# Kernel tuning notes

Hardware: AMD Instinct MI355X
Metric: run time of the kernel (lower is better)

Reference implementation:

```python
import jax, jax.numpy as jnp
import numpy as np

N_NODES = 100000
F_STATE = 64
HIDDEN = 256
N_EDGES = 1600000


def setup_inputs() -> dict:
    key = jax.random.key(0)
    ks = jax.random.split(key, 8)
    x = jax.random.normal(ks[0], (N_NODES, F_STATE), dtype=jnp.float32)
    edge_index = jax.random.randint(ks[1], (2, N_EDGES), 0, N_NODES, dtype=jnp.int32)
    # Pre-process MLP (1 layer): Dense(F_STATE -> HIDDEN), relu
    W_pre = jax.random.normal(ks[2], (F_STATE, HIDDEN), dtype=jnp.float32) / np.sqrt(F_STATE)
    b_pre = jnp.zeros((HIDDEN,), dtype=jnp.float32)
    # GeneralConv: Dense(HIDDEN -> HIDDEN), relu, then sum-aggregate message passing
    W_conv = jax.random.normal(ks[3], (HIDDEN, HIDDEN), dtype=jnp.float32) / np.sqrt(HIDDEN)
    b_conv = jnp.zeros((HIDDEN,), dtype=jnp.float32)
    # Post-process MLP (1 layer): Dense(2*HIDDEN -> F_STATE), activation=None
    W_post = jax.random.normal(ks[4], (2 * HIDDEN, F_STATE), dtype=jnp.float32) / np.sqrt(2 * HIDDEN)
    b_post = jnp.zeros((F_STATE,), dtype=jnp.float32)
    return {
        "x": x,
        "edge_index": edge_index,
        "W_pre": W_pre,
        "b_pre": b_pre,
        "W_conv": W_conv,
        "b_conv": b_conv,
        "W_post": W_post,
        "b_post": b_post,
        "steps": 4,
    }


def reference(x, edge_index, W_pre, b_pre, W_conv, b_conv, W_post, b_post, steps):
    n = x.shape[0]
    dst = edge_index[0]  # a.indices[:, 0] -> aggregation targets
    src = edge_index[1]  # a.indices[:, 1] -> message sources

    def step(h, _):
        p = jax.nn.relu(h @ W_pre + b_pre)                 # pre MLP     [N, H]
        m = jax.nn.relu(p @ W_conv + b_conv)               # conv dense  [N, H]
        z = jax.ops.segment_sum(m[src], dst, num_segments=n)  # sum agg  [N, H]
        out = jnp.concatenate([z, p], axis=-1) @ W_post + b_post  # cat-skip + post MLP (linear)
        return out, None

    out, _ = jax.lax.scan(step, x, None, length=steps)
    return out
```

## Files before the change

### kernel.cpp

```cpp
#include <hip/hip_runtime.h>


#define NN 100000
#define NPAD 100064
#define FS 64
#define HH 256
#define NE 1600000
#define NSTEPS 4
#define GA 128
#define EPB (NE / GA)
#define BK2SH 9
#define BS2 (1 << BK2SH)
#define NBK2 ((NN + BS2 - 1) / BS2)

typedef unsigned short u16;
typedef unsigned int u32;
typedef __attribute__((ext_vector_type(8))) short bfrag;
typedef __attribute__((ext_vector_type(4))) float ffrag;

static __device__ __forceinline__ u16 f2bf(float f) {
    union { float f; u32 u; } v; v.f = f;
    return (u16)((v.u + 0x7fffu + ((v.u >> 16) & 1u)) >> 16);
}
static __device__ __forceinline__ float bf2f(u16 h) {
    union { u32 u; float f; } v; v.u = (u32)h << 16; return v.f;
}
static __device__ __forceinline__ u32 pack2bf(float a, float b) {
    return (u32)f2bf(a) | ((u32)f2bf(b) << 16);
}

__global__ void cvt_x_k(const float4* __restrict__ x, uint2* __restrict__ hbf, int n4) {
    int i = blockIdx.x * 256 + threadIdx.x;
    if (i < n4) {
        float4 v = x[i];
        hbf[i] = make_uint2(pack2bf(v.x, v.y), pack2bf(v.z, v.w));
    }
}

__global__ void prep_w_k(const float* __restrict__ W_pre, const float* __restrict__ W_conv,
                         const float* __restrict__ W_post,
                         u16* __restrict__ Wpt, u16* __restrict__ Wct,
                         u16* __restrict__ Wzt, u16* __restrict__ Wp2t) {
    int i = blockIdx.x * 256 + threadIdx.x;
    if (i < 65536) {
        int c = i >> 8, k = i & 255;
        Wct[i] = f2bf(W_conv[k * HH + c]);
    } else if (i < 81920) {
        int j = i - 65536;
        int c = j >> 6, k = j & 63;
        Wpt[j] = f2bf(W_pre[k * HH + c]);
    } else if (i < 98304) {
        int j = i - 81920;
        int c = j >> 8, k = j & 255;
        Wzt[j] = f2bf(W_post[k * FS + c]);
    } else if (i < 114688) {
        int j = i - 98304;
        int c = j >> 8, k = j & 255;
        Wp2t[j] = f2bf(W_post[(HH + k) * FS + c]);
    }
}

__global__ __launch_bounds__(256) void fillA_k(const int* __restrict__ dst, const int* __restrict__ src,
                                               int* __restrict__ cntM, int* __restrict__ offM,
                                               u32* __restrict__ tmp) {
    __shared__ int cnt[256];
    __shared__ int sc[256];
    __shared__ int cur[256];
    const int t = threadIdx.x, b = blockIdx.x;
    const int e0 = b * EPB;
    cnt[t] = 0;
    __syncthreads();
    for (int i = t; i < EPB; i += 256) atomicAdd(&cnt[dst[e0 + i] >> BK2SH], 1);
    __syncthreads();
    int v = cnt[t];
    sc[t] = v;
    __syncthreads();
    for (int o = 1; o < 256; o <<= 1) {
        int y = (t >= o) ? sc[t - o] : 0;
        __syncthreads();
        sc[t] += y;
        __syncthreads();
    }
    int excl = sc[t] - v;
    cur[t] = excl;
    if (t < NBK2) {
        cntM[t * GA + b] = v;
        offM[t * GA + b] = excl;
    }
    __syncthreads();
    u32* seg = tmp + (size_t)b * EPB;
    for (int i = t; i < EPB; i += 256) {
        int d = dst[e0 + i], s = src[e0 + i];
        int pos = atomicAdd(&cur[d >> BK2SH], 1);
        seg[pos] = ((u32)(d & (BS2 - 1)) << 23) | (u32)s;
    }
}

__global__ void bscan_k(const int* __restrict__ cntM, int* __restrict__ bstart) {
    __shared__ int sh[256];
    const int t = threadIdx.x;
    int tot = 0;
    if (t < NBK2)
        for (int b = 0; b < GA; b++) tot += cntM[t * GA + b];
    sh[t] = tot;
    __syncthreads();
    for (int o = 1; o < 256; o <<= 1) {
        int y = (t >= o) ? sh[t - o] : 0;
        __syncthreads();
        sh[t] += y;
        __syncthreads();
    }
    if (t < NBK2) bstart[t] = sh[t] - tot;
    if (t == 255) bstart[NBK2] = sh[255];
}

__global__ __launch_bounds__(256) void fillB_k(const u32* __restrict__ tmp,
                                               const int* __restrict__ cntM, const int* __restrict__ offM,
                                               const int* __restrict__ bstart,
                                               int* __restrict__ offsets, int* __restrict__ srcs) {
    __shared__ int cnt[BS2];
    __shared__ int cur[BS2];
    __shared__ int runlen[GA];
    __shared__ int runoff[GA];
    const int t = threadIdx.x, k = blockIdx.x;
    const int nodeBase = k << BK2SH;
    cnt[t] = 0;
    cnt[t + 256] = 0;
    if (t < GA) {
        runlen[t] = cntM[k * GA + t];
        runoff[t] = offM[k * GA + t];
    }
    __syncthreads();
    const int rsub = t >> 6;
    const int elane = t & 63;
    for (int g = 0; g < GA / 4; g++) {
        int rb = g * 4 + rsub;
        int len = runlen[rb];
        const u32* run = tmp + (size_t)rb * EPB + runoff[rb];
        for (int e = elane; e < len; e += 64) atomicAdd(&cnt[run[e] >> 23], 1);
    }
    __syncthreads();
    int a = cnt[2 * t], b2 = cnt[2 * t + 1];
    int s = a + b2;
    cur[t] = s;
    __syncthreads();
    for (int o = 1; o < 256; o <<= 1) {
        int y = (t >= o) ? cur[t - o] : 0;
        __syncthreads();
        cur[t] += y;
        __syncthreads();
    }
    int exclPair = cur[t] - s;
    __syncthreads();
    const int base = bstart[k];
    int o0 = base + exclPair;
    int o1 = o0 + a;
    int n0 = nodeBase + 2 * t, n1 = n0 + 1;
    if (n0 < NN) offsets[n0] = o0;
    if (n1 < NN) offsets[n1] = o1;
    cur[2 * t] = o0;
    cur[2 * t + 1] = o1;
    __syncthreads();
    for (int g = 0; g < GA / 4; g++) {
        int rb = g * 4 + rsub;
        int len = runlen[rb];
        const u32* run = tmp + (size_t)rb * EPB + runoff[rb];
        for (int e = elane; e < len; e += 64) {
            u32 p = run[e];
            int pos = atomicAdd(&cur[p >> 23], 1);
            srcs[pos] = (int)(p & 0x7FFFFFu);
        }
    }
}

__global__ void final_off_k(int* __restrict__ offsets) {
    if (threadIdx.x == 0) offsets[NN] = NE;
}

__global__ __launch_bounds__(256, 3) void xform_k(const u16* __restrict__ hbf,
                                                  const u16* __restrict__ Wpt,
                                                  const float* __restrict__ b_pre,
                                                  const u16* __restrict__ Wct,
                                                  const float* __restrict__ b_conv,
                                                  const u16* __restrict__ Wzt,
                                                  const u16* __restrict__ Wp2t,
                                                  u16* __restrict__ qbf,
                                                  u16* __restrict__ pw2o) {
    __shared__ __align__(16) u16 ts[64 * 264];
    __shared__ __align__(16) u16 stA[64 * 72];
    __shared__ __align__(16) u16 stB[64 * 72];
    const int t = threadIdx.x;
    const int wave = t >> 6, lane = t & 63;
    const int quad = lane >> 4, l16 = lane & 15;
    const int nodeBase = blockIdx.x * 64;

    {
        ffrag acc[4][4];
#pragma unroll
        for (int mt = 0; mt < 4; mt++)
#pragma unroll
            for (int nt = 0; nt < 4; nt++) acc[mt][nt] = (ffrag)0.f;
#pragma unroll
        for (int ch = 0; ch < 2; ch++) {
            const int kb = ch * 32 + quad * 8;
            bfrag a[4], b[4];
#pragma unroll
            for (int mt = 0; mt < 4; mt++)
                a[mt] = *(const bfrag*)(hbf + (size_t)(nodeBase + mt * 16 + l16) * FS + kb);
#pragma unroll
            for (int nt = 0; nt < 4; nt++)
                b[nt] = *(const bfrag*)(Wpt + (size_t)(wave * 64 + nt * 16 + l16) * FS + kb);
#pragma unroll
            for (int mt = 0; mt < 4; mt++)
#pragma unroll
                for (int nt = 0; nt < 4; nt++)
                    acc[mt][nt] = __builtin_amdgcn_mfma_f32_16x16x32_bf16(a[mt], b[nt], acc[mt][nt], 0, 0, 0);
        }
#pragma unroll
        for (int nt = 0; nt < 4; nt++) {
            const int col = wave * 64 + nt * 16 + l16;
            const float bv = b_pre[col];
#pragma unroll
            for (int mt = 0; mt < 4; mt++)
#pragma unroll
                for (int r = 0; r < 4; r++)
                    ts[(mt * 16 + quad * 4 + r) * 264 + col] = f2bf(fmaxf(acc[mt][nt][r] + bv, 0.f));
        }
    }
    __syncthreads();

    ffrag accm[4][4];
    ffrag accw[4];
    {
#pragma unroll
        for (int mt = 0; mt < 4; mt++) {
            accw[mt] = (ffrag)0.f;
#pragma unroll
            for (int nt = 0; nt < 4; nt++) accm[mt][nt] = (ffrag)0.f;
        }
        bfrag b[2][4], bw[2];
        {
            const int kb0 = quad * 8;
#pragma unroll
            for (int nt = 0; nt < 4; nt++)
                b[0][nt] = *(const bfrag*)(Wct + (size_t)(wave * 64 + nt * 16 + l16) * HH + kb0);
            bw[0] = *(const bfrag*)(Wp2t + (size_t)(wave * 16 + l16) * HH + kb0);
        }
#pragma unroll
        for (int ch = 0; ch < 8; ch++) {
            const int cur = ch & 1, nxt = cur ^ 1;
            if (ch < 7) {
                const int kb2 = (ch + 1) * 32 + quad * 8;
#pragma unroll
                for (int nt = 0; nt < 4; nt++)
                    b[nxt][nt] = *(const bfrag*)(Wct + (size_t)(wave * 64 + nt * 16 + l16) * HH + kb2);
                bw[nxt] = *(const bfrag*)(Wp2t + (size_t)(wave * 16 + l16) * HH + kb2);
            }
            const int kb = ch * 32 + quad * 8;
            bfrag a[4];
#pragma unroll
            for (int mt = 0; mt < 4; mt++)
                a[mt] = *(const bfrag*)(ts + (mt * 16 + l16) * 264 + kb);
#pragma unroll
            for (int mt = 0; mt < 4; mt++) {
#pragma unroll
                for (int nt = 0; nt < 4; nt++)
                    accm[mt][nt] = __builtin_amdgcn_mfma_f32_16x16x32_bf16(a[mt], b[cur][nt], accm[mt][nt], 0, 0, 0);
                accw[mt] = __builtin_amdgcn_mfma_f32_16x16x32_bf16(a[mt], bw[cur], accw[mt], 0, 0, 0);
            }
        }
    }
    __syncthreads();

    {
#pragma unroll
        for (int nt = 0; nt < 4; nt++) {
            const int col = wave * 64 + nt * 16 + l16;
            const float bv = b_conv[col];
#pragma unroll
            for (int mt = 0; mt < 4; mt++)
#pragma unroll
                for (int r = 0; r < 4; r++)
                    ts[(mt * 16 + quad * 4 + r) * 264 + col] = f2bf(fmaxf(accm[mt][nt][r] + bv, 0.f));
        }
        const int colw = wave * 16 + l16;
#pragma unroll
        for (int mt = 0; mt < 4; mt++)
#pragma unroll
            for (int r = 0; r < 4; r++)
                stA[(mt * 16 + quad * 4 + r) * 72 + colw] = f2bf(accw[mt][r]);
    }
    __syncthreads();

#pragma unroll
    for (int s = 0; s < 2; s++) {
        const int j = t + s * 256;
        const int row = j >> 3, seg = j & 7;
        uint4 v = *(const uint4*)(stA + row * 72 + seg * 8);
        *(uint4*)(pw2o + (size_t)(nodeBase + row) * FS + seg * 8) = v;
    }

    {
        ffrag qa[4];
#pragma unroll
        for (int mt = 0; mt < 4; mt++) qa[mt] = (ffrag)0.f;
        bfrag bz[2];
        bz[0] = *(const bfrag*)(Wzt + (size_t)(wave * 16 + l16) * HH + quad * 8);
#pragma unroll
        for (int ch = 0; ch < 8; ch++) {
            const int cur = ch & 1;
            if (ch < 7)
                bz[cur ^ 1] = *(const bfrag*)(Wzt + (size_t)(wave * 16 + l16) * HH + (ch + 1) * 32 + quad * 8);
            const int kb = ch * 32 + quad * 8;
#pragma unroll
            for (int mt = 0; mt < 4; mt++) {
                bfrag am = *(const bfrag*)(ts + (mt * 16 + l16) * 264 + kb);
                qa[mt] = __builtin_amdgcn_mfma_f32_16x16x32_bf16(am, bz[cur], qa[mt], 0, 0, 0);
            }
        }
        const int col = wave * 16 + l16;
#pragma unroll
        for (int mt = 0; mt < 4; mt++)
#pragma unroll
            for (int r = 0; r < 4; r++)
                stB[(mt * 16 + quad * 4 + r) * 72 + col] = f2bf(qa[mt][r]);
    }
    __syncthreads();

#pragma unroll
    for (int s = 0; s < 2; s++) {
        const int j = t + s * 256;
        const int row = j >> 3, seg = j & 7;
        uint4 v = *(const uint4*)(stB + row * 72 + seg * 8);
        *(uint4*)(qbf + (size_t)(nodeBase + row) * FS + seg * 8) = v;
    }
}

__global__ __launch_bounds__(256) void agg_k(const u32* __restrict__ q2,
                                             const int* __restrict__ offsets,
                                             const int* __restrict__ srcs,
                                             const u32* __restrict__ pw2,
                                             const float* __restrict__ b_post,
                                             u32* __restrict__ hbf_out,
                                             float* __restrict__ outf) {
    const int wave = threadIdx.x >> 6;
    const int lane = threadIdx.x & 63;
    const int node = blockIdx.x * 4 + wave;
    const int half = lane >> 5, c = lane & 31;
    const int beg = offsets[node], end = offsets[node + 1];
    float ax = 0.f, ay = 0.f, bx = 0.f, by = 0.f;
    int e = beg + half;
    for (; e + 6 < end; e += 8) {
        int s0 = srcs[e], s1 = srcs[e + 2], s2 = srcs[e + 4], s3 = srcs[e + 6];
        u32 g0 = q2[(size_t)s0 * 32 + c];
        u32 g1 = q2[(size_t)s1 * 32 + c];
        u32 g2 = q2[(size_t)s2 * 32 + c];
        u32 g3 = q2[(size_t)s3 * 32 + c];
        ax += bf2f((u16)g0) + bf2f((u16)g1);
        ay += bf2f((u16)(g0 >> 16)) + bf2f((u16)(g1 >> 16));
        bx += bf2f((u16)g2) + bf2f((u16)g3);
        by += bf2f((u16)(g2 >> 16)) + bf2f((u16)(g3 >> 16));
    }
    for (; e < end; e += 2) {
        u32 g = q2[(size_t)srcs[e] * 32 + c];
        ax += bf2f((u16)g);
        ay += bf2f((u16)(g >> 16));
    }
    ax += bx; ay += by;
    ax += __shfl_xor(ax, 32);
    ay += __shfl_xor(ay, 32);
    if (half == 0) {
        u32 wp = pw2[(size_t)node * 32 + c];
        float2 b = *(const float2*)&b_post[2 * c];
        float hx = ax + bf2f((u16)wp) + b.x;
        float hy = ay + bf2f((u16)(wp >> 16)) + b.y;
        if (outf) {
            *(float2*)&outf[(size_t)node * FS + 2 * c] = make_float2(hx, hy);
        } else {
            hbf_out[(size_t)node * 32 + c] = pack2bf(hx, hy);
        }
    }
}

extern "C" void kernel_launch(void* const* d_in, const int* in_sizes, int n_in,
                              void* d_out, int out_size, void* d_ws, size_t ws_size,
                              hipStream_t stream) {
    const float* x      = (const float*)d_in[0];
    const int*   ei     = (const int*)d_in[1];
    const float* W_pre  = (const float*)d_in[2];
    const float* b_pre  = (const float*)d_in[3];
    const float* W_conv = (const float*)d_in[4];
    const float* b_conv = (const float*)d_in[5];
    const float* W_post = (const float*)d_in[6];
    const float* b_post = (const float*)d_in[7];
    float* out = (float*)d_out;

    char* ws = (char*)d_ws;
    size_t off = 0;
    auto alloc = [&](size_t bytes) -> char* {
        char* r = ws + off;
        off += (bytes + 255) & ~(size_t)255;
        return r;
    };
    u16* hbf     = (u16*)alloc((size_t)NPAD * FS * 2);
    u16* qbf     = (u16*)alloc((size_t)NPAD * FS * 2);
    u16* pw2     = (u16*)alloc((size_t)NPAD * FS * 2);
    u32* tmp     = (u32*)alloc((size_t)NE * 4);
    int* offsets = (int*)alloc((size_t)(NN + 1) * 4);
    int* srcs    = (int*)alloc((size_t)NE * 4);
    int* cntM    = (int*)alloc((size_t)NBK2 * GA * 4);
    int* offM    = (int*)alloc((size_t)NBK2 * GA * 4);
    int* bstart  = (int*)alloc((size_t)(NBK2 + 1) * 4);
    u16* Wpt     = (u16*)alloc((size_t)HH * FS * 2);
    u16* Wct     = (u16*)alloc((size_t)HH * HH * 2);
    u16* Wzt     = (u16*)alloc((size_t)FS * HH * 2);
    u16* Wp2t    = (u16*)alloc((size_t)FS * HH * 2);
    (void)ws_size; (void)in_sizes; (void)n_in; (void)out_size;

    const int* dst = ei;
    const int* src = ei + NE;

    cvt_x_k<<<(NN * FS / 4 + 255) / 256, 256, 0, stream>>>((const float4*)x, (uint2*)hbf, NN * FS / 4);
    prep_w_k<<<448, 256, 0, stream>>>(W_pre, W_conv, W_post, Wpt, Wct, Wzt, Wp2t);

    fillA_k<<<GA, 256, 0, stream>>>(dst, src, cntM, offM, tmp);
    bscan_k<<<1, 256, 0, stream>>>(cntM, bstart);
    fillB_k<<<NBK2, 256, 0, stream>>>(tmp, cntM, offM, bstart, offsets, srcs);
    final_off_k<<<1, 64, 0, stream>>>(offsets);

    const int GB = (NN + 63) / 64;
    for (int s = 0; s < NSTEPS; s++) {
        xform_k<<<GB, 256, 0, stream>>>(hbf, Wpt, b_pre, Wct, b_conv, Wzt, Wp2t, qbf, pw2);
        if (s < NSTEPS - 1)
            agg_k<<<NN / 4, 256, 0, stream>>>((const u32*)qbf, offsets, srcs, (const u32*)pw2, b_post,
                                              (u32*)hbf, nullptr);
        else
            agg_k<<<NN / 4, 256, 0, stream>>>((const u32*)qbf, offsets, srcs, (const u32*)pw2, b_post,
                                              nullptr, out);
    }
}
```

Baseline: 607.6 us.

## Split xform tile across eight waves and deepen gather unroll in aggregation

The node-transform kernel moves from 4 to 8 waves per 64-node block. Each wave now computes 32 output columns instead of 64, and the small 64-wide projections are split by row-tile and column-half. This lowers per-wave register pressure and raises occupancy, but it drops the explicit double-buffered weight prefetch and adds a barrier around the shared staging buffer, which is now reused. The aggregation kernel also gains a 16-edge unrolled loop so more independent gathers are in flight per half-wave.

```diff
diff --git a/kernel.cpp b/kernel.cpp
--- a/kernel.cpp
+++ b/kernel.cpp
@@ -177,7 +177,7 @@
     if (threadIdx.x == 0) offsets[NN] = NE;
 }
 
-__global__ __launch_bounds__(256, 3) void xform_k(const u16* __restrict__ hbf,
+__global__ __launch_bounds__(512, 4) void xform_k(const u16* __restrict__ hbf,
                                                   const u16* __restrict__ Wpt,
                                                   const float* __restrict__ b_pre,
                                                   const u16* __restrict__ Wct,
@@ -187,38 +187,39 @@
                                                   u16* __restrict__ qbf,
                                                   u16* __restrict__ pw2o) {
     __shared__ __align__(16) u16 ts[64 * 264];
-    __shared__ __align__(16) u16 stA[64 * 72];
-    __shared__ __align__(16) u16 stB[64 * 72];
+    __shared__ __align__(16) u16 st[64 * 72];
     const int t = threadIdx.x;
     const int wave = t >> 6, lane = t & 63;
     const int quad = lane >> 4, l16 = lane & 15;
+    const int w4 = wave & 3;
+    const int wh = wave >> 2;
     const int nodeBase = blockIdx.x * 64;
 
     {
-        ffrag acc[4][4];
-#pragma unroll
-        for (int mt = 0; mt < 4; mt++)
-#pragma unroll
-            for (int nt = 0; nt < 4; nt++) acc[mt][nt] = (ffrag)0.f;
+        ffrag acc[4][2];
+#pragma unroll
+        for (int mt = 0; mt < 4; mt++) {
+            acc[mt][0] = (ffrag)0.f;
+            acc[mt][1] = (ffrag)0.f;
+        }
 #pragma unroll
         for (int ch = 0; ch < 2; ch++) {
             const int kb = ch * 32 + quad * 8;
-            bfrag a[4], b[4];
+            bfrag a[4], b0, b1;
 #pragma unroll
             for (int mt = 0; mt < 4; mt++)
                 a[mt] = *(const bfrag*)(hbf + (size_t)(nodeBase + mt * 16 + l16) * FS + kb);
-#pragma unroll
-            for (int nt = 0; nt < 4; nt++)
-                b[nt] = *(const bfrag*)(Wpt + (size_t)(wave * 64 + nt * 16 + l16) * FS + kb);
-#pragma unroll
-            for (int mt = 0; mt < 4; mt++)
-#pragma unroll
-                for (int nt = 0; nt < 4; nt++)
-                    acc[mt][nt] = __builtin_amdgcn_mfma_f32_16x16x32_bf16(a[mt], b[nt], acc[mt][nt], 0, 0, 0);
-        }
-#pragma unroll
-        for (int nt = 0; nt < 4; nt++) {
-            const int col = wave * 64 + nt * 16 + l16;
+            b0 = *(const bfrag*)(Wpt + (size_t)(wave * 32 + l16) * FS + kb);
+            b1 = *(const bfrag*)(Wpt + (size_t)(wave * 32 + 16 + l16) * FS + kb);
+#pragma unroll
+            for (int mt = 0; mt < 4; mt++) {
+                acc[mt][0] = __builtin_amdgcn_mfma_f32_16x16x32_bf16(a[mt], b0, acc[mt][0], 0, 0, 0);
+                acc[mt][1] = __builtin_amdgcn_mfma_f32_16x16x32_bf16(a[mt], b1, acc[mt][1], 0, 0, 0);
+            }
+        }
+#pragma unroll
+        for (int nt = 0; nt < 2; nt++) {
+            const int col = wave * 32 + nt * 16 + l16;
             const float bv = b_pre[col];
 #pragma unroll
             for (int mt = 0; mt < 4; mt++)
@@ -229,53 +230,43 @@
     }
     __syncthreads();
 
-    ffrag accm[4][4];
-    ffrag accw[4];
+    ffrag accm[4][2];
+    ffrag accw[2];
     {
 #pragma unroll
         for (int mt = 0; mt < 4; mt++) {
-            accw[mt] = (ffrag)0.f;
-#pragma unroll
-            for (int nt = 0; nt < 4; nt++) accm[mt][nt] = (ffrag)0.f;
-        }
-        bfrag b[2][4], bw[2];
-        {
-            const int kb0 = quad * 8;
-#pragma unroll
-            for (int nt = 0; nt < 4; nt++)
-                b[0][nt] = *(const bfrag*)(Wct + (size_t)(wave * 64 + nt * 16 + l16) * HH + kb0);
-            bw[0] = *(const bfrag*)(Wp2t + (size_t)(wave * 16 + l16) * HH + kb0);
-        }
+            accm[mt][0] = (ffrag)0.f;
+            accm[mt][1] = (ffrag)0.f;
+        }
+        accw[0] = (ffrag)0.f;
+        accw[1] = (ffrag)0.f;
 #pragma unroll
         for (int ch = 0; ch < 8; ch++) {
-            const int cur = ch & 1, nxt = cur ^ 1;
-            if (ch < 7) {
-                const int kb2 = (ch + 1) * 32 + quad * 8;
-#pragma unroll
-                for (int nt = 0; nt < 4; nt++)
-                    b[nxt][nt] = *(const bfrag*)(Wct + (size_t)(wave * 64 + nt * 16 + l16) * HH + kb2);
-                bw[nxt] = *(const bfrag*)(Wp2t + (size_t)(wave * 16 + l16) * HH + kb2);
-            }
             const int kb = ch * 32 + quad * 8;
             bfrag a[4];
 #pragma unroll
             for (int mt = 0; mt < 4; mt++)
                 a[mt] = *(const bfrag*)(ts + (mt * 16 + l16) * 264 + kb);
+            bfrag aw = *(const bfrag*)(ts + (w4 * 16 + l16) * 264 + kb);
+            bfrag b0 = *(const bfrag*)(Wct + (size_t)(wave * 32 + l16) * HH + kb);
+            bfrag b1 = *(const bfrag*)(Wct + (size_t)(wave * 32 + 16 + l16) * HH + kb);
+            bfrag bw0 = *(const bfrag*)(Wp2t + (size_t)(wh * 32 + l16) * HH + kb);
+            bfrag bw1 = *(const bfrag*)(Wp2t + (size_t)(wh * 32 + 16 + l16) * HH + kb);
 #pragma unroll
             for (int mt = 0; mt < 4; mt++) {
-#pragma unroll
-                for (int nt = 0; nt < 4; nt++)
-                    accm[mt][nt] = __builtin_amdgcn_mfma_f32_16x16x32_bf16(a[mt], b[cur][nt], accm[mt][nt], 0, 0, 0);
-                accw[mt] = __builtin_amdgcn_mfma_f32_16x16x32_bf16(a[mt], bw[cur], accw[mt], 0, 0, 0);
+                accm[mt][0] = __builtin_amdgcn_mfma_f32_16x16x32_bf16(a[mt], b0, accm[mt][0], 0, 0, 0);
+                accm[mt][1] = __builtin_amdgcn_mfma_f32_16x16x32_bf16(a[mt], b1, accm[mt][1], 0, 0, 0);
             }
-        }
-    }
-    __syncthreads();
-
-    {
-#pragma unroll
-        for (int nt = 0; nt < 4; nt++) {
-            const int col = wave * 64 + nt * 16 + l16;
+            accw[0] = __builtin_amdgcn_mfma_f32_16x16x32_bf16(aw, bw0, accw[0], 0, 0, 0);
+            accw[1] = __builtin_amdgcn_mfma_f32_16x16x32_bf16(aw, bw1, accw[1], 0, 0, 0);
+        }
+    }
+    __syncthreads();
+
+    {
+#pragma unroll
+        for (int nt = 0; nt < 2; nt++) {
+            const int col = wave * 32 + nt * 16 + l16;
             const float bv = b_conv[col];
 #pragma unroll
             for (int mt = 0; mt < 4; mt++)
@@ -283,55 +274,45 @@
                 for (int r = 0; r < 4; r++)
                     ts[(mt * 16 + quad * 4 + r) * 264 + col] = f2bf(fmaxf(accm[mt][nt][r] + bv, 0.f));
         }
-        const int colw = wave * 16 + l16;
-#pragma unroll
-        for (int mt = 0; mt < 4; mt++)
+#pragma unroll
+        for (int nt = 0; nt < 2; nt++)
 #pragma unroll
             for (int r = 0; r < 4; r++)
-                stA[(mt * 16 + quad * 4 + r) * 72 + colw] = f2bf(accw[mt][r]);
-    }
-    __syncthreads();
-
-#pragma unroll
-    for (int s = 0; s < 2; s++) {
-        const int j = t + s * 256;
-        const int row = j >> 3, seg = j & 7;
-        uint4 v = *(const uint4*)(stA + row * 72 + seg * 8);
+                st[(w4 * 16 + quad * 4 + r) * 72 + wh * 32 + nt * 16 + l16] = f2bf(accw[nt][r]);
+    }
+    __syncthreads();
+
+    {
+        const int row = t >> 3, seg = t & 7;
+        uint4 v = *(const uint4*)(st + row * 72 + seg * 8);
         *(uint4*)(pw2o + (size_t)(nodeBase + row) * FS + seg * 8) = v;
     }
-
-    {
-        ffrag qa[4];
-#pragma unroll
-        for (int mt = 0; mt < 4; mt++) qa[mt] = (ffrag)0.f;
-        bfrag bz[2];
-        bz[0] = *(const bfrag*)(Wzt + (size_t)(wave * 16 + l16) * HH + quad * 8);
+    __syncthreads();
+
+    {
+        ffrag qa[2];
+        qa[0] = (ffrag)0.f;
+        qa[1] = (ffrag)0.f;
 #pragma unroll
         for (int ch = 0; ch < 8; ch++) {
-            const int cur = ch & 1;
-            if (ch < 7)
-                bz[cur ^ 1] = *(const bfrag*)(Wzt + (size_t)(wave * 16 + l16) * HH + (ch + 1) * 32 + quad * 8);
             const int kb = ch * 32 + quad * 8;
-#pragma unroll
-            for (int mt = 0; mt < 4; mt++) {
-                bfrag am = *(const bfrag*)(ts + (mt * 16 + l16) * 264 + kb);
-                qa[mt] = __builtin_amdgcn_mfma_f32_16x16x32_bf16(am, bz[cur], qa[mt], 0, 0, 0);
-            }
-        }
-        const int col = wave * 16 + l16;
-#pragma unroll
-        for (int mt = 0; mt < 4; mt++)
+            bfrag am = *(const bfrag*)(ts + (w4 * 16 + l16) * 264 + kb);
+            bfrag bz0 = *(const bfrag*)(Wzt + (size_t)(wh * 32 + l16) * HH + kb);
+            bfrag bz1 = *(const bfrag*)(Wzt + (size_t)(wh * 32 + 16 + l16) * HH + kb);
+            qa[0] = __builtin_amdgcn_mfma_f32_16x16x32_bf16(am, bz0, qa[0], 0, 0, 0);
+            qa[1] = __builtin_amdgcn_mfma_f32_16x16x32_bf16(am, bz1, qa[1], 0, 0, 0);
+        }
+#pragma unroll
+        for (int nt = 0; nt < 2; nt++)
 #pragma unroll
             for (int r = 0; r < 4; r++)
-                stB[(mt * 16 + quad * 4 + r) * 72 + col] = f2bf(qa[mt][r]);
-    }
-    __syncthreads();
-
-#pragma unroll
-    for (int s = 0; s < 2; s++) {
-        const int j = t + s * 256;
-        const int row = j >> 3, seg = j & 7;
-        uint4 v = *(const uint4*)(stB + row * 72 + seg * 8);
+                st[(w4 * 16 + quad * 4 + r) * 72 + wh * 32 + nt * 16 + l16] = f2bf(qa[nt][r]);
+    }
+    __syncthreads();
+
+    {
+        const int row = t >> 3, seg = t & 7;
+        uint4 v = *(const uint4*)(st + row * 72 + seg * 8);
         *(uint4*)(qbf + (size_t)(nodeBase + row) * FS + seg * 8) = v;
     }
 }
@@ -350,6 +331,22 @@
     const int beg = offsets[node], end = offsets[node + 1];
     float ax = 0.f, ay = 0.f, bx = 0.f, by = 0.f;
     int e = beg + half;
+    for (; e + 14 < end; e += 16) {
+        int s0 = srcs[e], s1 = srcs[e + 2], s2 = srcs[e + 4], s3 = srcs[e + 6];
+        int s4 = srcs[e + 8], s5 = srcs[e + 10], s6 = srcs[e + 12], s7 = srcs[e + 14];
+        u32 g0 = q2[(size_t)s0 * 32 + c];
+        u32 g1 = q2[(size_t)s1 * 32 + c];
+        u32 g2 = q2[(size_t)s2 * 32 + c];
+        u32 g3 = q2[(size_t)s3 * 32 + c];
+        u32 g4 = q2[(size_t)s4 * 32 + c];
+        u32 g5 = q2[(size_t)s5 * 32 + c];
+        u32 g6 = q2[(size_t)s6 * 32 + c];
+        u32 g7 = q2[(size_t)s7 * 32 + c];
+        ax += bf2f((u16)g0) + bf2f((u16)g1) + bf2f((u16)g4) + bf2f((u16)g5);
+        ay += bf2f((u16)(g0 >> 16)) + bf2f((u16)(g1 >> 16)) + bf2f((u16)(g4 >> 16)) + bf2f((u16)(g5 >> 16));
+        bx += bf2f((u16)g2) + bf2f((u16)g3) + bf2f((u16)g6) + bf2f((u16)g7);
+        by += bf2f((u16)(g2 >> 16)) + bf2f((u16)(g3 >> 16)) + bf2f((u16)(g6 >> 16)) + bf2f((u16)(g7 >> 16));
+    }
     for (; e + 6 < end; e += 8) {
         int s0 = srcs[e], s1 = srcs[e + 2], s2 = srcs[e + 4], s3 = srcs[e + 6];
         u32 g0 = q2[(size_t)s0 * 32 + c];
@@ -430,7 +427,7 @@
 
     const int GB = (NN + 63) / 64;
     for (int s = 0; s < NSTEPS; s++) {
-        xform_k<<<GB, 256, 0, stream>>>(hbf, Wpt, b_pre, Wct, b_conv, Wzt, Wp2t, qbf, pw2);
+        xform_k<<<GB, 512, 0, stream>>>(hbf, Wpt, b_pre, Wct, b_conv, Wzt, Wp2t, qbf, pw2);
         if (s < NSTEPS - 1)
             agg_k<<<NN / 4, 256, 0, stream>>>((const u32*)qbf, offsets, srcs, (const u32*)pw2, b_post,
                                               (u32*)hbf, nullptr);
```

After: 762.1 us. 25.4% more time.

## Stage conv and post weights into LDS via async global_load_lds with swizzle

Applied to the files above, without the earlier changes.

The second GEMM in xform_k now brings W_conv and W_post weight chunks into shared memory with global_load_lds, using an XOR swizzle, and one block-wide copy per k-chunk. Before, each wave read its own weight fragments from global memory with register double buffering. The aim is to cut redundant global/L2 traffic and register pressure, and to let the next chunk's load overlap the MFMAs. It adds two block barriers per chunk and reuses one staging buffer for the outputs, which reduces LDS footprint and may help occupancy.

```diff
diff --git a/kernel.cpp b/kernel.cpp
--- a/kernel.cpp
+++ b/kernel.cpp
@@ -12,6 +12,7 @@
 #define BK2SH 9
 #define BS2 (1 << BK2SH)
 #define NBK2 ((NN + BS2 - 1) / BS2)
+#define WSTB 33792
 
 typedef unsigned short u16;
 typedef unsigned int u32;
@@ -27,6 +28,11 @@
 }
 static __device__ __forceinline__ u32 pack2bf(float a, float b) {
     return (u32)f2bf(a) | ((u32)f2bf(b) << 16);
+}
+
+static __device__ __forceinline__ void gload16(const void* g, void* l) {
+    __builtin_amdgcn_global_load_lds((const __attribute__((address_space(1))) void*)g,
+                                     (__attribute__((address_space(3))) void*)l, 16, 0, 0);
 }
 
 __global__ void cvt_x_k(const float4* __restrict__ x, uint2* __restrict__ hbf, int n4) {
@@ -177,6 +183,23 @@
     if (threadIdx.x == 0) offsets[NN] = NE;
 }
 
+static __device__ __forceinline__ void stage2w(const u16* __restrict__ Wct,
+                                               const u16* __restrict__ Wp2t,
+                                               char* smem, int t, int ch) {
+#pragma unroll
+    for (int call = 0; call < 5; call++) {
+        const int idx = call * 256 + t;
+        const int row = idx >> 2;
+        const int slot = t & 3;
+        const int sw = (row >> 1) & 3;
+        const int ku = ch * 32 + ((slot ^ sw) << 3);
+        const u16* g = (row < 256) ? (Wct + (size_t)row * HH + ku)
+                                   : (Wp2t + (size_t)(row - 256) * HH + ku);
+        void* l = smem + WSTB + call * 4096 + (t & ~63) * 16;
+        gload16(g, l);
+    }
+}
+
 __global__ __launch_bounds__(256, 3) void xform_k(const u16* __restrict__ hbf,
                                                   const u16* __restrict__ Wpt,
                                                   const float* __restrict__ b_pre,
@@ -186,14 +209,17 @@
                                                   const u16* __restrict__ Wp2t,
                                                   u16* __restrict__ qbf,
                                                   u16* __restrict__ pw2o) {
-    __shared__ __align__(16) u16 ts[64 * 264];
-    __shared__ __align__(16) u16 stA[64 * 72];
-    __shared__ __align__(16) u16 stB[64 * 72];
+    __shared__ __align__(16) char smem[WSTB + 20480];
+    u16* ts = (u16*)smem;
+    u16* st = (u16*)(smem + WSTB);
+    const char* wstc = smem + WSTB;
     const int t = threadIdx.x;
     const int wave = t >> 6, lane = t & 63;
     const int quad = lane >> 4, l16 = lane & 15;
     const int nodeBase = blockIdx.x * 64;
 
+    stage2w(Wct, Wp2t, smem, t, 0);
+
     {
         ffrag acc[4][4];
 #pragma unroll
@@ -227,7 +253,6 @@
                     ts[(mt * 16 + quad * 4 + r) * 264 + col] = f2bf(fmaxf(acc[mt][nt][r] + bv, 0.f));
         }
     }
-    __syncthreads();
 
     ffrag accm[4][4];
     ffrag accw[4];
@@ -238,35 +263,27 @@
 #pragma unroll
             for (int nt = 0; nt < 4; nt++) accm[mt][nt] = (ffrag)0.f;
         }
-        bfrag b[2][4], bw[2];
-        {
-            const int kb0 = quad * 8;
+        const int swb = ((l16 >> 1) & 3) << 4;
+#pragma unroll
+        for (int ch = 0; ch < 8; ch++) {
+            __syncthreads();
+            const int kb = ch * 32 + quad * 8;
+            bfrag a[4], b[4], bw;
 #pragma unroll
             for (int nt = 0; nt < 4; nt++)
-                b[0][nt] = *(const bfrag*)(Wct + (size_t)(wave * 64 + nt * 16 + l16) * HH + kb0);
-            bw[0] = *(const bfrag*)(Wp2t + (size_t)(wave * 16 + l16) * HH + kb0);
-        }
-#pragma unroll
-        for (int ch = 0; ch < 8; ch++) {
-            const int cur = ch & 1, nxt = cur ^ 1;
-            if (ch < 7) {
-                const int kb2 = (ch + 1) * 32 + quad * 8;
-#pragma unroll
-                for (int nt = 0; nt < 4; nt++)
-                    b[nxt][nt] = *(const bfrag*)(Wct + (size_t)(wave * 64 + nt * 16 + l16) * HH + kb2);
-                bw[nxt] = *(const bfrag*)(Wp2t + (size_t)(wave * 16 + l16) * HH + kb2);
-            }
-            const int kb = ch * 32 + quad * 8;
-            bfrag a[4];
+                b[nt] = *(const bfrag*)(wstc + (wave * 64 + nt * 16 + l16) * 64 + ((quad << 4) ^ swb));
+            bw = *(const bfrag*)(wstc + (256 + wave * 16 + l16) * 64 + ((quad << 4) ^ swb));
 #pragma unroll
             for (int mt = 0; mt < 4; mt++)
                 a[mt] = *(const bfrag*)(ts + (mt * 16 + l16) * 264 + kb);
+            __syncthreads();
+            if (ch < 7) stage2w(Wct, Wp2t, smem, t, ch + 1);
 #pragma unroll
             for (int mt = 0; mt < 4; mt++) {
 #pragma unroll
                 for (int nt = 0; nt < 4; nt++)
-                    accm[mt][nt] = __builtin_amdgcn_mfma_f32_16x16x32_bf16(a[mt], b[cur][nt], accm[mt][nt], 0, 0, 0);
-                accw[mt] = __builtin_amdgcn_mfma_f32_16x16x32_bf16(a[mt], bw[cur], accw[mt], 0, 0, 0);
+                    accm[mt][nt] = __builtin_amdgcn_mfma_f32_16x16x32_bf16(a[mt], b[nt], accm[mt][nt], 0, 0, 0);
+                accw[mt] = __builtin_amdgcn_mfma_f32_16x16x32_bf16(a[mt], bw, accw[mt], 0, 0, 0);
             }
         }
     }
@@ -288,7 +305,7 @@
         for (int mt = 0; mt < 4; mt++)
 #pragma unroll
             for (int r = 0; r < 4; r++)
-                stA[(mt * 16 + quad * 4 + r) * 72 + colw] = f2bf(accw[mt][r]);
+                st[(mt * 16 + quad * 4 + r) * 72 + colw] = f2bf(accw[mt][r]);
     }
     __syncthreads();
 
@@ -296,9 +313,10 @@
     for (int s = 0; s < 2; s++) {
         const int j = t + s * 256;
         const int row = j >> 3, seg = j & 7;
-        uint4 v = *(const uint4*)(stA + row * 72 + seg * 8);
+        uint4 v = *(const uint4*)(st + row * 72 + seg * 8);
         *(uint4*)(pw2o + (size_t)(nodeBase + row) * FS + seg * 8) = v;
     }
+    __syncthreads();
 
     {
         ffrag qa[4];
@@ -323,7 +341,7 @@
         for (int mt = 0; mt < 4; mt++)
 #pragma unroll
             for (int r = 0; r < 4; r++)
-                stB[(mt * 16 + quad * 4 + r) * 72 + col] = f2bf(qa[mt][r]);
+                st[(mt * 16 + quad * 4 + r) * 72 + col] = f2bf(qa[mt][r]);
     }
     __syncthreads();
 
@@ -331,7 +349,7 @@
     for (int s = 0; s < 2; s++) {
         const int j = t + s * 256;
         const int row = j >> 3, seg = j & 7;
-        uint4 v = *(const uint4*)(stB + row * 72 + seg * 8);
+        uint4 v = *(const uint4*)(st + row * 72 + seg * 8);
         *(uint4*)(qbf + (size_t)(nodeBase + row) * FS + seg * 8) = v;
     }
 }
```

Measured after the change: 608.6 us. Within noise of the previous version (+0.2%).
